# Optimization experiments

Measured on AMD Instinct MI355X. Metric: run time of the kernel, lower is better.

Reference implementation:

```python
import jax, jax.numpy as jnp
import numpy as np

N_NODES = 50000
N_EDGES = 800000
F_IN = 128
HEADS = 4
C_OUT = 16
NEG_SLOPE = 0.2


def setup_inputs() -> dict:
    key = jax.random.key(0)
    k1, k2, k3, k4, k5 = jax.random.split(key, 5)
    x = jax.random.normal(k1, (N_NODES, F_IN), dtype=jnp.float32)
    edge_index = jax.random.randint(k2, (2, N_EDGES), 0, N_NODES, dtype=jnp.int64)
    W = jax.random.normal(k3, (F_IN, HEADS * C_OUT), dtype=jnp.float32) * (1.0 / np.sqrt(F_IN))
    att_src = jax.random.normal(k4, (HEADS, C_OUT), dtype=jnp.float32) * (1.0 / np.sqrt(C_OUT))
    att_dst = jax.random.normal(k5, (HEADS, C_OUT), dtype=jnp.float32) * (1.0 / np.sqrt(C_OUT))
    bias = jnp.zeros((HEADS * C_OUT,), dtype=jnp.float32)
    return {"x": x, "edge_index": edge_index, "W": W,
            "att_src": att_src, "att_dst": att_dst, "bias": bias}


def reference(x, edge_index, W, att_src, att_dst, bias):
    N = x.shape[0]
    H, C = att_src.shape
    # PyG GATConv default: add self-loops
    loop = jnp.arange(N, dtype=edge_index.dtype)
    ei = jnp.concatenate([edge_index, jnp.stack([loop, loop])], axis=1)  # [2, E+N]
    src, dst = ei[0], ei[1]

    h = (x @ W).reshape(N, H, C)                      # [N, H, C]
    a_src = jnp.einsum('nhc,hc->nh', h, att_src)      # [N, H]
    a_dst = jnp.einsum('nhc,hc->nh', h, att_dst)      # [N, H]

    e = a_src[src] + a_dst[dst]                       # [E+N, H]
    e = jnp.where(e > 0, e, NEG_SLOPE * e)            # leaky_relu(0.2)

    # segment softmax over destination node (every segment has a self-loop)
    m = jax.ops.segment_max(e, dst, num_segments=N)   # [N, H]
    e = jnp.exp(e - m[dst])
    s = jax.ops.segment_sum(e, dst, num_segments=N)   # [N, H]
    alpha = e / (s[dst] + 1e-16)                      # [E+N, H]

    # scatter-aggregate weighted neighbor features
    out = jax.ops.segment_sum(h[src] * alpha[..., None], dst, num_segments=N)  # [N, H, C]
    out = out.reshape(N, H * C) + bias                # concat heads + bias
    return out, alpha
```

## Files before the change

### kernel.cpp

```cpp
#include <hip/hip_runtime.h>

#define N_NODES 50000
#define N_EDGES 800000
#define EN      (N_EDGES + N_NODES)
#define F_IN    128
#define HC      64
#define NEG_SLOPE 0.2f
#define NBUCK   196
#define BCAP    5120
#define P3_EPB  4096
#define LIN_BLOCKS 782
#define NBLK    196
#define RCAP    64
#define NSLOT   (NBLK * RCAP)
#define XPAD    136

typedef __attribute__((ext_vector_type(8))) short bf16x8;
typedef __attribute__((ext_vector_type(4))) float f32x4;

static __device__ __forceinline__ unsigned short f2bf(float f) {
    unsigned int b = __float_as_uint(f);
    return (unsigned short)((b + 0x7FFFu + ((b >> 16) & 1u)) >> 16);
}

__global__ __launch_bounds__(256) void
kA_linear_bin(const float* __restrict__ x, const float* __restrict__ W,
              const float* __restrict__ att_src, const float* __restrict__ att_dst,
              const int* __restrict__ ei,
              unsigned short* __restrict__ hbf, float* __restrict__ a_src,
              float* __restrict__ a_dst, int* __restrict__ bins,
              int* __restrict__ cntg) {
    __shared__ unsigned short xs[64][XPAD];
    __shared__ unsigned short wt[80][XPAD];
    __shared__ int bcnt_l[NBUCK];
    const int tid = threadIdx.x;

    if (blockIdx.x >= LIN_BLOCKS) {
        const int blk = blockIdx.x - LIN_BLOCKS;
        for (int i = tid; i < NBUCK; i += 256) bcnt_l[i] = 0;
        __syncthreads();
        const int base = blk * P3_EPB;
        #pragma unroll
        for (int j = 0; j < 16; ++j) {
            int i = base + j * 256 + tid;
            if (i < N_EDGES) {
                int sv = ei[i];
                int d  = ei[N_EDGES + i];
                int bk = d >> 8;
                int r  = atomicAdd(&bcnt_l[bk], 1);
                if (r < RCAP)
                    bins[(bk * NBLK + blk) * RCAP + r] = sv | ((d & 255) << 16);
            }
        }
        __syncthreads();
        for (int b = tid; b < NBUCK; b += 256)
            cntg[b * NBLK + blk] = min(bcnt_l[b], RCAP);
        return;
    }

    const int wv   = tid >> 6;
    const int l    = tid & 63;
    const int base = blockIdx.x * 64;
    const int c16  = l & 15;
    const int grp  = l >> 4;

    #pragma unroll
    for (int it = 0; it < 8; ++it) {
        int f  = it * 1024 + tid * 4;
        int k  = f >> 6;
        int cl = f & 63;
        float4 v = *(const float4*)(W + (size_t)k * HC + cl);
        wt[cl + 0][k] = f2bf(v.x);
        wt[cl + 1][k] = f2bf(v.y);
        wt[cl + 2][k] = f2bf(v.z);
        wt[cl + 3][k] = f2bf(v.w);
    }

    #pragma unroll
    for (int it = 0; it < 8; ++it) {
        int f   = it * 1024 + tid * 4;
        int row = f >> 7, k = f & 127;
        int gr  = base + row;
        float4 v = {0.f, 0.f, 0.f, 0.f};
        if (gr < N_NODES) v = *(const float4*)(x + (size_t)gr * F_IN + k);
        ushort4 u = {f2bf(v.x), f2bf(v.y), f2bf(v.z), f2bf(v.w)};
        *(ushort4*)(&xs[row][k]) = u;
    }

    {
        const int wk = tid >> 1;
        const int wo = (tid & 1) * 4;
        const float* wrow = W + (size_t)wk * HC;
        #pragma unroll
        for (int oo = 0; oo < 4; ++oo) {
            const int o = wo + oo;
            const int h = o & 3;
            const float* av = (o < 4) ? (att_src + h * 16) : (att_dst + h * 16);
            float a = 0.f;
            #pragma unroll
            for (int c = 0; c < 16; c += 4) {
                float4 w4 = *(const float4*)(wrow + h * 16 + c);
                float4 a4 = *(const float4*)(av + c);
                a += w4.x * a4.x + w4.y * a4.y + w4.z * a4.z + w4.w * a4.w;
            }
            wt[64 + o][wk] = f2bf(a);
        }
    }
    __syncthreads();

    bf16x8 Bf[5][4];
    #pragma unroll
    for (int t = 0; t < 5; ++t)
        #pragma unroll
        for (int kk = 0; kk < 4; ++kk)
            Bf[t][kk] = *(const bf16x8*)(&wt[t * 16 + c16][kk * 32 + grp * 8]);

    const int r0 = wv * 16;
    f32x4 C[4], C4;
    #pragma unroll
    for (int t = 0; t < 4; ++t) C[t] = (f32x4){0.f, 0.f, 0.f, 0.f};
    C4 = (f32x4){0.f, 0.f, 0.f, 0.f};
    bf16x8 A[4];
    #pragma unroll
    for (int kk = 0; kk < 4; ++kk)
        A[kk] = *(const bf16x8*)(&xs[r0 + c16][kk * 32 + grp * 8]);
    #pragma unroll
    for (int t = 0; t < 4; ++t)
        #pragma unroll
        for (int kk = 0; kk < 4; ++kk)
            C[t] = __builtin_amdgcn_mfma_f32_16x16x32_bf16(A[kk], Bf[t][kk], C[t], 0, 0, 0);
    #pragma unroll
    for (int kk = 0; kk < 4; ++kk)
        C4 = __builtin_amdgcn_mfma_f32_16x16x32_bf16(A[kk], Bf[4][kk], C4, 0, 0, 0);

    #pragma unroll
    for (int j = 0; j < 4; ++j) {
        const int row = base + r0 + grp * 4 + j;
        if (row < N_NODES) {
            #pragma unroll
            for (int t = 0; t < 4; ++t)
                hbf[(size_t)row * HC + t * 16 + c16] = f2bf(C[t][j]);
            if (c16 < 4)      a_src[row * 4 + c16]       = C4[j];
            else if (c16 < 8) a_dst[row * 4 + (c16 - 4)] = C4[j];
        }
    }
}

__global__ __launch_bounds__(256) void
p4_csr(const int* __restrict__ bins, const int* __restrict__ cntg,
       int* __restrict__ row_info, int* __restrict__ srcs) {
    __shared__ int psum[256];
    __shared__ int cnt[256], sm[256], cur[256];
    const int b = blockIdx.x, tid = threadIdx.x;
    const int node = (b << 8) + tid;

    psum[tid] = (tid < NBLK) ? cntg[b * NBLK + tid] : 0;
    cnt[tid] = (node < N_NODES) ? 1 : 0;
    __syncthreads();
    for (int off = 1; off < 256; off <<= 1) {
        int t = (tid >= off) ? psum[tid - off] : 0;
        __syncthreads();
        psum[tid] += t;
        __syncthreads();
    }
    const int T = psum[255];
    const int* bb = bins + (size_t)b * NSLOT;

    int pvs[20];
    #pragma unroll
    for (int it = 0; it < 20; ++it) {
        const int i = tid + it * 256;
        if (i < T) {
            int lo = 0, hi = NBLK - 1;
            while (lo < hi) { int mid = (lo + hi) >> 1;
                              if (psum[mid] > i) hi = mid; else lo = mid + 1; }
            const int k  = i - (lo ? psum[lo - 1] : 0);
            const int pv = bb[lo * RCAP + k];
            pvs[it] = pv;
            atomicAdd(&cnt[pv >> 16], 1);
        }
    }
    __syncthreads();

    int v = cnt[tid];
    sm[tid] = v;
    __syncthreads();
    for (int off = 1; off < 256; off <<= 1) {
        int t = (tid >= off) ? sm[tid - off] : 0;
        __syncthreads();
        sm[tid] += t;
        __syncthreads();
    }
    const int ex = sm[tid] - v;
    const int sbase = b * BCAP;

    if (node < N_NODES) {
        row_info[node] = ((sbase + ex) << 8) | v;
        srcs[sbase + ex] = node;
    }
    cur[tid] = ex + 1;
    __syncthreads();
    #pragma unroll
    for (int it = 0; it < 20; ++it) {
        const int i = tid + it * 256;
        if (i < T) {
            const int pv = pvs[it];
            const int p  = atomicAdd(&cur[pv >> 16], 1);
            srcs[sbase + p] = pv & 0xFFFF;
        }
    }
}

__global__ __launch_bounds__(256) void
k_agg(const int* __restrict__ row_info, const int* __restrict__ srcs,
      const float* __restrict__ a_src, const float* __restrict__ a_dst,
      const unsigned int* __restrict__ hw,
      const float* __restrict__ bias, float* __restrict__ out,
      float* __restrict__ s_inv) {
    __shared__ int   s_lds[4][4][16];
    __shared__ float p_lds[4][4][16][4];

    const int tid  = threadIdx.x;
    const int wv   = tid >> 6;
    const int lane = tid & 63;
    const int g    = lane >> 4;
    const int l    = lane & 15;
    const int hd   = l >> 2;
    const int d    = blockIdx.x * 16 + wv * 4 + g;

    const int info   = row_info[d];
    const int begin  = info >> 8;
    const int cnt    = info & 255;
    const int nchunk = (cnt + 15) >> 4;
    const float4 ad  = *(const float4*)(a_dst + d * 4);

    float4 ps = {0.f, 0.f, 0.f, 0.f};
    float a0 = 0.f, a1 = 0.f, a2 = 0.f, a3 = 0.f;

    for (int c = 0; c < nchunk; ++c) {
        const int k0 = begin + c * 16;
        const int m  = min(16, begin + cnt - k0);
        const int s = srcs[k0 + (l < m ? l : m - 1)];
        float4 p = {0.f, 0.f, 0.f, 0.f};
        if (l < m) {
            float4 as = *(const float4*)(a_src + s * 4);
            float e0 = as.x + ad.x, e1 = as.y + ad.y, e2 = as.z + ad.z, e3 = as.w + ad.w;
            e0 = e0 > 0.f ? e0 : NEG_SLOPE * e0;
            e1 = e1 > 0.f ? e1 : NEG_SLOPE * e1;
            e2 = e2 > 0.f ? e2 : NEG_SLOPE * e2;
            e3 = e3 > 0.f ? e3 : NEG_SLOPE * e3;
            p.x = __expf(e0); p.y = __expf(e1); p.z = __expf(e2); p.w = __expf(e3);
            ps.x += p.x; ps.y += p.y; ps.z += p.z; ps.w += p.w;
        }
        s_lds[wv][g][l] = s;
        *(float4*)(&p_lds[wv][g][l][0]) = p;
        __threadfence_block();

        const int mp = (m + 3) & ~3;
        for (int e = 0; e < mp; e += 4) {
            int s0 = s_lds[wv][g][e + 0], s1 = s_lds[wv][g][e + 1];
            int s2 = s_lds[wv][g][e + 2], s3 = s_lds[wv][g][e + 3];
            float p0 = p_lds[wv][g][e + 0][hd], p1 = p_lds[wv][g][e + 1][hd];
            float p2 = p_lds[wv][g][e + 2][hd], p3 = p_lds[wv][g][e + 3][hd];
            uint2 u0 = *(const uint2*)(hw + (size_t)s0 * 32 + l * 2);
            uint2 u1 = *(const uint2*)(hw + (size_t)s1 * 32 + l * 2);
            uint2 u2 = *(const uint2*)(hw + (size_t)s2 * 32 + l * 2);
            uint2 u3 = *(const uint2*)(hw + (size_t)s3 * 32 + l * 2);
            a0 += __uint_as_float(u0.x << 16)         * p0;
            a1 += __uint_as_float(u0.x & 0xFFFF0000u) * p0;
            a2 += __uint_as_float(u0.y << 16)         * p0;
            a3 += __uint_as_float(u0.y & 0xFFFF0000u) * p0;
            a0 += __uint_as_float(u1.x << 16)         * p1;
            a1 += __uint_as_float(u1.x & 0xFFFF0000u) * p1;
            a2 += __uint_as_float(u1.y << 16)         * p1;
            a3 += __uint_as_float(u1.y & 0xFFFF0000u) * p1;
            a0 += __uint_as_float(u2.x << 16)         * p2;
            a1 += __uint_as_float(u2.x & 0xFFFF0000u) * p2;
            a2 += __uint_as_float(u2.y << 16)         * p2;
            a3 += __uint_as_float(u2.y & 0xFFFF0000u) * p2;
            a0 += __uint_as_float(u3.x << 16)         * p3;
            a1 += __uint_as_float(u3.x & 0xFFFF0000u) * p3;
            a2 += __uint_as_float(u3.y << 16)         * p3;
            a3 += __uint_as_float(u3.y & 0xFFFF0000u) * p3;
        }
        __threadfence_block();
    }

    #pragma unroll
    for (int mm = 1; mm < 16; mm <<= 1) {
        ps.x += __shfl_xor(ps.x, mm);
        ps.y += __shfl_xor(ps.y, mm);
        ps.z += __shfl_xor(ps.z, mm);
        ps.w += __shfl_xor(ps.w, mm);
    }
    const float4 inv = {1.f / (ps.x + 1e-16f), 1.f / (ps.y + 1e-16f),
                        1.f / (ps.z + 1e-16f), 1.f / (ps.w + 1e-16f)};
    if (l == 0) *(float4*)(s_inv + d * 4) = inv;

    const float invh = (hd == 0) ? inv.x : (hd == 1) ? inv.y : (hd == 2) ? inv.z : inv.w;
    float4 o;
    o.x = a0 * invh + bias[l * 4 + 0];
    o.y = a1 * invh + bias[l * 4 + 1];
    o.z = a2 * invh + bias[l * 4 + 2];
    o.w = a3 * invh + bias[l * 4 + 3];
    *(float4*)(out + (size_t)d * HC + l * 4) = o;
}

__global__ void k_alpha(const int* __restrict__ ei, const float* __restrict__ a_src,
                        const float* __restrict__ a_dst, const float* __restrict__ s_inv,
                        float* __restrict__ alpha_out) {
    int i2 = blockIdx.x * 256 + threadIdx.x;
    if (i2 >= EN / 2) return;
    const int i = i2 * 2;
    int s0, s1, d0, d1;
    if (i < N_EDGES) {
        int2 sp = *(const int2*)(ei + i);
        int2 dp = *(const int2*)(ei + N_EDGES + i);
        s0 = sp.x; s1 = sp.y; d0 = dp.x; d1 = dp.y;
    } else {
        s0 = d0 = i - N_EDGES;
        s1 = d1 = i + 1 - N_EDGES;
    }

    float4 as0 = *(const float4*)(a_src + s0 * 4);
    float4 ad0 = *(const float4*)(a_dst + d0 * 4);
    float4 iv0 = *(const float4*)(s_inv + d0 * 4);
    float4 as1 = *(const float4*)(a_src + s1 * 4);
    float4 ad1 = *(const float4*)(a_dst + d1 * 4);
    float4 iv1 = *(const float4*)(s_inv + d1 * 4);

    float e0, e1, e2, e3;
    e0 = as0.x + ad0.x; e1 = as0.y + ad0.y; e2 = as0.z + ad0.z; e3 = as0.w + ad0.w;
    e0 = e0 > 0.f ? e0 : NEG_SLOPE * e0;
    e1 = e1 > 0.f ? e1 : NEG_SLOPE * e1;
    e2 = e2 > 0.f ? e2 : NEG_SLOPE * e2;
    e3 = e3 > 0.f ? e3 : NEG_SLOPE * e3;
    float4 al0 = {__expf(e0) * iv0.x, __expf(e1) * iv0.y,
                  __expf(e2) * iv0.z, __expf(e3) * iv0.w};
    e0 = as1.x + ad1.x; e1 = as1.y + ad1.y; e2 = as1.z + ad1.z; e3 = as1.w + ad1.w;
    e0 = e0 > 0.f ? e0 : NEG_SLOPE * e0;
    e1 = e1 > 0.f ? e1 : NEG_SLOPE * e1;
    e2 = e2 > 0.f ? e2 : NEG_SLOPE * e2;
    e3 = e3 > 0.f ? e3 : NEG_SLOPE * e3;
    float4 al1 = {__expf(e0) * iv1.x, __expf(e1) * iv1.y,
                  __expf(e2) * iv1.z, __expf(e3) * iv1.w};

    *(float4*)(alpha_out + (size_t)i * 4)     = al0;
    *(float4*)(alpha_out + (size_t)i * 4 + 4) = al1;
}

extern "C" void kernel_launch(void* const* d_in, const int* in_sizes, int n_in,
                              void* d_out, int out_size, void* d_ws, size_t ws_size,
                              hipStream_t stream) {
    const float* x       = (const float*)d_in[0];
    const int*   ei      = (const int*)d_in[1];
    const float* W       = (const float*)d_in[2];
    const float* att_src = (const float*)d_in[3];
    const float* att_dst = (const float*)d_in[4];
    const float* bias    = (const float*)d_in[5];

    float* out       = (float*)d_out;
    float* alpha_out = (float*)d_out + (size_t)N_NODES * HC;

    char* ws = (char*)d_ws;
    size_t off = 0;
    unsigned short* hbf = (unsigned short*)(ws + off); off += (size_t)N_NODES * HC * 2;
    float* a_src   = (float*)(ws + off); off += (size_t)N_NODES * 4 * 4;
    float* a_dst   = (float*)(ws + off); off += (size_t)N_NODES * 4 * 4;
    float* s_inv   = (float*)(ws + off); off += (size_t)N_NODES * 4 * 4;
    int* row_info  = (int*)(ws + off);   off += (size_t)N_NODES * 4;
    int* srcs      = (int*)(ws + off);   off += (size_t)NBUCK * BCAP * 4;
    int* bins      = (int*)(ws + off);   off += (size_t)NBUCK * NSLOT * 4;
    int* cntg      = (int*)(ws + off);   off += (size_t)NBUCK * NBLK * 4;

    kA_linear_bin<<<LIN_BLOCKS + NBLK, 256, 0, stream>>>(x, W, att_src, att_dst, ei,
                                                         hbf, a_src, a_dst, bins, cntg);
    p4_csr<<<NBUCK, 256, 0, stream>>>(bins, cntg, row_info, srcs);
    k_agg<<<N_NODES / 16, 256, 0, stream>>>(row_info, srcs, a_src, a_dst,
                                            (const unsigned int*)hbf, bias, out, s_inv);
    k_alpha<<<(EN / 2 + 255) / 256, 256, 0, stream>>>(ei, a_src, a_dst, s_inv, alpha_out);
}
```

Measured before the change: 80.93 us.

## Fuse alpha computation into aggregation kernel by storing edge ids in CSR

```diff
diff --git a/kernel.cpp b/kernel.cpp
--- a/kernel.cpp
+++ b/kernel.cpp
@@ -44,12 +44,11 @@
         for (int j = 0; j < 16; ++j) {
             int i = base + j * 256 + tid;
             if (i < N_EDGES) {
-                int sv = ei[i];
                 int d  = ei[N_EDGES + i];
                 int bk = d >> 8;
                 int r  = atomicAdd(&bcnt_l[bk], 1);
                 if (r < RCAP)
-                    bins[(bk * NBLK + blk) * RCAP + r] = sv | ((d & 255) << 16);
+                    bins[(bk * NBLK + blk) * RCAP + r] = i | ((d & 255) << 24);
             }
         }
         __syncthreads();
@@ -148,7 +147,7 @@
 
 __global__ __launch_bounds__(256) void
 p4_csr(const int* __restrict__ bins, const int* __restrict__ cntg,
-       int* __restrict__ row_info, int* __restrict__ srcs) {
+       int* __restrict__ row_info, int* __restrict__ eids) {
     __shared__ int psum[256];
     __shared__ int cnt[256], sm[256], cur[256];
     const int b = blockIdx.x, tid = threadIdx.x;
@@ -177,7 +176,7 @@
             const int k  = i - (lo ? psum[lo - 1] : 0);
             const int pv = bb[lo * RCAP + k];
             pvs[it] = pv;
-            atomicAdd(&cnt[pv >> 16], 1);
+            atomicAdd(&cnt[((unsigned)pv) >> 24], 1);
         }
     }
     __syncthreads();
@@ -196,7 +195,7 @@
 
     if (node < N_NODES) {
         row_info[node] = ((sbase + ex) << 8) | v;
-        srcs[sbase + ex] = node;
+        eids[sbase + ex] = N_EDGES + node;
     }
     cur[tid] = ex + 1;
     __syncthreads();
@@ -205,18 +204,19 @@
         const int i = tid + it * 256;
         if (i < T) {
             const int pv = pvs[it];
-            const int p  = atomicAdd(&cur[pv >> 16], 1);
-            srcs[sbase + p] = pv & 0xFFFF;
+            const int p  = atomicAdd(&cur[((unsigned)pv) >> 24], 1);
+            eids[sbase + p] = pv & 0xFFFFFF;
         }
     }
 }
 
 __global__ __launch_bounds__(256) void
-k_agg(const int* __restrict__ row_info, const int* __restrict__ srcs,
+k_agg(const int* __restrict__ row_info, const int* __restrict__ eids,
+      const int* __restrict__ ei,
       const float* __restrict__ a_src, const float* __restrict__ a_dst,
       const unsigned int* __restrict__ hw,
       const float* __restrict__ bias, float* __restrict__ out,
-      float* __restrict__ s_inv) {
+      float* __restrict__ alpha_out) {
     __shared__ int   s_lds[4][4][16];
     __shared__ float p_lds[4][4][16][4];
 
@@ -240,7 +240,8 @@
     for (int c = 0; c < nchunk; ++c) {
         const int k0 = begin + c * 16;
         const int m  = min(16, begin + cnt - k0);
-        const int s = srcs[k0 + (l < m ? l : m - 1)];
+        const int eid = eids[k0 + (l < m ? l : m - 1)];
+        const int s   = (eid >= N_EDGES) ? (eid - N_EDGES) : ei[eid];
         float4 p = {0.f, 0.f, 0.f, 0.f};
         if (l < m) {
             float4 as = *(const float4*)(a_src + s * 4);
@@ -295,7 +296,6 @@
     }
     const float4 inv = {1.f / (ps.x + 1e-16f), 1.f / (ps.y + 1e-16f),
                         1.f / (ps.z + 1e-16f), 1.f / (ps.w + 1e-16f)};
-    if (l == 0) *(float4*)(s_inv + d * 4) = inv;
 
     const float invh = (hd == 0) ? inv.x : (hd == 1) ? inv.y : (hd == 2) ? inv.z : inv.w;
     float4 o;
@@ -304,49 +304,24 @@
     o.z = a2 * invh + bias[l * 4 + 2];
     o.w = a3 * invh + bias[l * 4 + 3];
     *(float4*)(out + (size_t)d * HC + l * 4) = o;
-}
-
-__global__ void k_alpha(const int* __restrict__ ei, const float* __restrict__ a_src,
-                        const float* __restrict__ a_dst, const float* __restrict__ s_inv,
-                        float* __restrict__ alpha_out) {
-    int i2 = blockIdx.x * 256 + threadIdx.x;
-    if (i2 >= EN / 2) return;
-    const int i = i2 * 2;
-    int s0, s1, d0, d1;
-    if (i < N_EDGES) {
-        int2 sp = *(const int2*)(ei + i);
-        int2 dp = *(const int2*)(ei + N_EDGES + i);
-        s0 = sp.x; s1 = sp.y; d0 = dp.x; d1 = dp.y;
-    } else {
-        s0 = d0 = i - N_EDGES;
-        s1 = d1 = i + 1 - N_EDGES;
-    }
-
-    float4 as0 = *(const float4*)(a_src + s0 * 4);
-    float4 ad0 = *(const float4*)(a_dst + d0 * 4);
-    float4 iv0 = *(const float4*)(s_inv + d0 * 4);
-    float4 as1 = *(const float4*)(a_src + s1 * 4);
-    float4 ad1 = *(const float4*)(a_dst + d1 * 4);
-    float4 iv1 = *(const float4*)(s_inv + d1 * 4);
-
-    float e0, e1, e2, e3;
-    e0 = as0.x + ad0.x; e1 = as0.y + ad0.y; e2 = as0.z + ad0.z; e3 = as0.w + ad0.w;
-    e0 = e0 > 0.f ? e0 : NEG_SLOPE * e0;
-    e1 = e1 > 0.f ? e1 : NEG_SLOPE * e1;
-    e2 = e2 > 0.f ? e2 : NEG_SLOPE * e2;
-    e3 = e3 > 0.f ? e3 : NEG_SLOPE * e3;
-    float4 al0 = {__expf(e0) * iv0.x, __expf(e1) * iv0.y,
-                  __expf(e2) * iv0.z, __expf(e3) * iv0.w};
-    e0 = as1.x + ad1.x; e1 = as1.y + ad1.y; e2 = as1.z + ad1.z; e3 = as1.w + ad1.w;
-    e0 = e0 > 0.f ? e0 : NEG_SLOPE * e0;
-    e1 = e1 > 0.f ? e1 : NEG_SLOPE * e1;
-    e2 = e2 > 0.f ? e2 : NEG_SLOPE * e2;
-    e3 = e3 > 0.f ? e3 : NEG_SLOPE * e3;
-    float4 al1 = {__expf(e0) * iv1.x, __expf(e1) * iv1.y,
-                  __expf(e2) * iv1.z, __expf(e3) * iv1.w};
-
-    *(float4*)(alpha_out + (size_t)i * 4)     = al0;
-    *(float4*)(alpha_out + (size_t)i * 4 + 4) = al1;
+
+    for (int c = 0; c < nchunk; ++c) {
+        const int k0 = begin + c * 16;
+        const int m  = min(16, begin + cnt - k0);
+        if (l < m) {
+            const int eid = eids[k0 + l];
+            const int s   = (eid >= N_EDGES) ? (eid - N_EDGES) : ei[eid];
+            float4 as = *(const float4*)(a_src + s * 4);
+            float e0 = as.x + ad.x, e1 = as.y + ad.y, e2 = as.z + ad.z, e3 = as.w + ad.w;
+            e0 = e0 > 0.f ? e0 : NEG_SLOPE * e0;
+            e1 = e1 > 0.f ? e1 : NEG_SLOPE * e1;
+            e2 = e2 > 0.f ? e2 : NEG_SLOPE * e2;
+            e3 = e3 > 0.f ? e3 : NEG_SLOPE * e3;
+            float4 al = {__expf(e0) * inv.x, __expf(e1) * inv.y,
+                         __expf(e2) * inv.z, __expf(e3) * inv.w};
+            *(float4*)(alpha_out + (size_t)eid * 4) = al;
+        }
+    }
 }
 
 extern "C" void kernel_launch(void* const* d_in, const int* in_sizes, int n_in,
@@ -367,16 +342,14 @@
     unsigned short* hbf = (unsigned short*)(ws + off); off += (size_t)N_NODES * HC * 2;
     float* a_src   = (float*)(ws + off); off += (size_t)N_NODES * 4 * 4;
     float* a_dst   = (float*)(ws + off); off += (size_t)N_NODES * 4 * 4;
-    float* s_inv   = (float*)(ws + off); off += (size_t)N_NODES * 4 * 4;
     int* row_info  = (int*)(ws + off);   off += (size_t)N_NODES * 4;
-    int* srcs      = (int*)(ws + off);   off += (size_t)NBUCK * BCAP * 4;
+    int* eids      = (int*)(ws + off);   off += (size_t)NBUCK * BCAP * 4;
     int* bins      = (int*)(ws + off);   off += (size_t)NBUCK * NSLOT * 4;
     int* cntg      = (int*)(ws + off);   off += (size_t)NBUCK * NBLK * 4;
 
     kA_linear_bin<<<LIN_BLOCKS + NBLK, 256, 0, stream>>>(x, W, att_src, att_dst, ei,
                                                          hbf, a_src, a_dst, bins, cntg);
-    p4_csr<<<NBUCK, 256, 0, stream>>>(bins, cntg, row_info, srcs);
-    k_agg<<<N_NODES / 16, 256, 0, stream>>>(row_info, srcs, a_src, a_dst,
-                                            (const unsigned int*)hbf, bias, out, s_inv);
-    k_alpha<<<(EN / 2 + 255) / 256, 256, 0, stream>>>(ei, a_src, a_dst, s_inv, alpha_out);
-}
+    p4_csr<<<NBUCK, 256, 0, stream>>>(bins, cntg, row_info, eids);
+    k_agg<<<N_NODES / 16, 256, 0, stream>>>(row_info, eids, ei, a_src, a_dst,
+                                            (const unsigned int*)hbf, bias, out, alpha_out);
+}
```

New measurement: 90.45 us. +11.8%, slower.

## Assign one wavefront per destination node in aggregation kernel

Applied to the files above, without the earlier changes.

```diff
diff --git a/kernel.cpp b/kernel.cpp
--- a/kernel.cpp
+++ b/kernel.cpp
@@ -217,32 +217,31 @@
       const unsigned int* __restrict__ hw,
       const float* __restrict__ bias, float* __restrict__ out,
       float* __restrict__ s_inv) {
-    __shared__ int   s_lds[4][4][16];
-    __shared__ float p_lds[4][4][16][4];
+    __shared__ int   s_l[4][64];
+    __shared__ float p_l[4][64][4];
 
     const int tid  = threadIdx.x;
     const int wv   = tid >> 6;
     const int lane = tid & 63;
-    const int g    = lane >> 4;
-    const int l    = lane & 15;
-    const int hd   = l >> 2;
-    const int d    = blockIdx.x * 16 + wv * 4 + g;
-
-    const int info   = row_info[d];
-    const int begin  = info >> 8;
-    const int cnt    = info & 255;
-    const int nchunk = (cnt + 15) >> 4;
-    const float4 ad  = *(const float4*)(a_dst + d * 4);
+    const int g16  = lane >> 4;
+    const int c16  = lane & 15;
+    const int hd   = c16 >> 2;
+    const int d    = blockIdx.x * 4 + wv;
+
+    const int info  = row_info[d];
+    const int begin = info >> 8;
+    const int cnt   = info & 255;
+    const float4 ad = *(const float4*)(a_dst + d * 4);
 
     float4 ps = {0.f, 0.f, 0.f, 0.f};
     float a0 = 0.f, a1 = 0.f, a2 = 0.f, a3 = 0.f;
 
-    for (int c = 0; c < nchunk; ++c) {
-        const int k0 = begin + c * 16;
-        const int m  = min(16, begin + cnt - k0);
-        const int s = srcs[k0 + (l < m ? l : m - 1)];
+    for (int c0 = 0; c0 < cnt; c0 += 64) {
+        const int m = min(64, cnt - c0);
+        int s = d;
         float4 p = {0.f, 0.f, 0.f, 0.f};
-        if (l < m) {
+        if (lane < m) {
+            s = srcs[begin + c0 + lane];
             float4 as = *(const float4*)(a_src + s * 4);
             float e0 = as.x + ad.x, e1 = as.y + ad.y, e2 = as.z + ad.z, e3 = as.w + ad.w;
             e0 = e0 > 0.f ? e0 : NEG_SLOPE * e0;
@@ -252,42 +251,46 @@
             p.x = __expf(e0); p.y = __expf(e1); p.z = __expf(e2); p.w = __expf(e3);
             ps.x += p.x; ps.y += p.y; ps.z += p.z; ps.w += p.w;
         }
-        s_lds[wv][g][l] = s;
-        *(float4*)(&p_lds[wv][g][l][0]) = p;
+        s_l[wv][lane] = s;
+        *(float4*)(&p_l[wv][lane][0]) = p;
         __threadfence_block();
 
-        const int mp = (m + 3) & ~3;
-        for (int e = 0; e < mp; e += 4) {
-            int s0 = s_lds[wv][g][e + 0], s1 = s_lds[wv][g][e + 1];
-            int s2 = s_lds[wv][g][e + 2], s3 = s_lds[wv][g][e + 3];
-            float p0 = p_lds[wv][g][e + 0][hd], p1 = p_lds[wv][g][e + 1][hd];
-            float p2 = p_lds[wv][g][e + 2][hd], p3 = p_lds[wv][g][e + 3][hd];
-            uint2 u0 = *(const uint2*)(hw + (size_t)s0 * 32 + l * 2);
-            uint2 u1 = *(const uint2*)(hw + (size_t)s1 * 32 + l * 2);
-            uint2 u2 = *(const uint2*)(hw + (size_t)s2 * 32 + l * 2);
-            uint2 u3 = *(const uint2*)(hw + (size_t)s3 * 32 + l * 2);
-            a0 += __uint_as_float(u0.x << 16)         * p0;
-            a1 += __uint_as_float(u0.x & 0xFFFF0000u) * p0;
-            a2 += __uint_as_float(u0.y << 16)         * p0;
-            a3 += __uint_as_float(u0.y & 0xFFFF0000u) * p0;
-            a0 += __uint_as_float(u1.x << 16)         * p1;
-            a1 += __uint_as_float(u1.x & 0xFFFF0000u) * p1;
-            a2 += __uint_as_float(u1.y << 16)         * p1;
-            a3 += __uint_as_float(u1.y & 0xFFFF0000u) * p1;
-            a0 += __uint_as_float(u2.x << 16)         * p2;
-            a1 += __uint_as_float(u2.x & 0xFFFF0000u) * p2;
-            a2 += __uint_as_float(u2.y << 16)         * p2;
-            a3 += __uint_as_float(u2.y & 0xFFFF0000u) * p2;
-            a0 += __uint_as_float(u3.x << 16)         * p3;
-            a1 += __uint_as_float(u3.x & 0xFFFF0000u) * p3;
-            a2 += __uint_as_float(u3.y << 16)         * p3;
-            a3 += __uint_as_float(u3.y & 0xFFFF0000u) * p3;
+        const int mp16 = (m + 15) & ~15;
+        #pragma unroll
+        for (int eb = 0; eb < 4; ++eb) {
+            const int e = eb * 16;
+            if (e < mp16) {
+                int sA = s_l[wv][e + 0  + g16], sB = s_l[wv][e + 4  + g16];
+                int sC = s_l[wv][e + 8  + g16], sD = s_l[wv][e + 12 + g16];
+                float pA = p_l[wv][e + 0  + g16][hd], pB = p_l[wv][e + 4  + g16][hd];
+                float pC = p_l[wv][e + 8  + g16][hd], pD = p_l[wv][e + 12 + g16][hd];
+                uint2 uA = *(const uint2*)(hw + (size_t)sA * 32 + c16 * 2);
+                uint2 uB = *(const uint2*)(hw + (size_t)sB * 32 + c16 * 2);
+                uint2 uC = *(const uint2*)(hw + (size_t)sC * 32 + c16 * 2);
+                uint2 uD = *(const uint2*)(hw + (size_t)sD * 32 + c16 * 2);
+                a0 += __uint_as_float(uA.x << 16)         * pA;
+                a1 += __uint_as_float(uA.x & 0xFFFF0000u) * pA;
+                a2 += __uint_as_float(uA.y << 16)         * pA;
+                a3 += __uint_as_float(uA.y & 0xFFFF0000u) * pA;
+                a0 += __uint_as_float(uB.x << 16)         * pB;
+                a1 += __uint_as_float(uB.x & 0xFFFF0000u) * pB;
+                a2 += __uint_as_float(uB.y << 16)         * pB;
+                a3 += __uint_as_float(uB.y & 0xFFFF0000u) * pB;
+                a0 += __uint_as_float(uC.x << 16)         * pC;
+                a1 += __uint_as_float(uC.x & 0xFFFF0000u) * pC;
+                a2 += __uint_as_float(uC.y << 16)         * pC;
+                a3 += __uint_as_float(uC.y & 0xFFFF0000u) * pC;
+                a0 += __uint_as_float(uD.x << 16)         * pD;
+                a1 += __uint_as_float(uD.x & 0xFFFF0000u) * pD;
+                a2 += __uint_as_float(uD.y << 16)         * pD;
+                a3 += __uint_as_float(uD.y & 0xFFFF0000u) * pD;
+            }
         }
         __threadfence_block();
     }
 
     #pragma unroll
-    for (int mm = 1; mm < 16; mm <<= 1) {
+    for (int mm = 1; mm < 64; mm <<= 1) {
         ps.x += __shfl_xor(ps.x, mm);
         ps.y += __shfl_xor(ps.y, mm);
         ps.z += __shfl_xor(ps.z, mm);
@@ -295,15 +298,23 @@
     }
     const float4 inv = {1.f / (ps.x + 1e-16f), 1.f / (ps.y + 1e-16f),
                         1.f / (ps.z + 1e-16f), 1.f / (ps.w + 1e-16f)};
-    if (l == 0) *(float4*)(s_inv + d * 4) = inv;
-
-    const float invh = (hd == 0) ? inv.x : (hd == 1) ? inv.y : (hd == 2) ? inv.z : inv.w;
-    float4 o;
-    o.x = a0 * invh + bias[l * 4 + 0];
-    o.y = a1 * invh + bias[l * 4 + 1];
-    o.z = a2 * invh + bias[l * 4 + 2];
-    o.w = a3 * invh + bias[l * 4 + 3];
-    *(float4*)(out + (size_t)d * HC + l * 4) = o;
+    if (lane == 0) *(float4*)(s_inv + d * 4) = inv;
+
+    a0 += __shfl_xor(a0, 16); a0 += __shfl_xor(a0, 32);
+    a1 += __shfl_xor(a1, 16); a1 += __shfl_xor(a1, 32);
+    a2 += __shfl_xor(a2, 16); a2 += __shfl_xor(a2, 32);
+    a3 += __shfl_xor(a3, 16); a3 += __shfl_xor(a3, 32);
+
+    if (g16 == 0) {
+        const float invh = (hd == 0) ? inv.x : (hd == 1) ? inv.y
+                         : (hd == 2) ? inv.z : inv.w;
+        float4 o;
+        o.x = a0 * invh + bias[c16 * 4 + 0];
+        o.y = a1 * invh + bias[c16 * 4 + 1];
+        o.z = a2 * invh + bias[c16 * 4 + 2];
+        o.w = a3 * invh + bias[c16 * 4 + 3];
+        *(float4*)(out + (size_t)d * HC + c16 * 4) = o;
+    }
 }
 
 __global__ void k_alpha(const int* __restrict__ ei, const float* __restrict__ a_src,
@@ -376,7 +387,7 @@
     kA_linear_bin<<<LIN_BLOCKS + NBLK, 256, 0, stream>>>(x, W, att_src, att_dst, ei,
                                                          hbf, a_src, a_dst, bins, cntg);
     p4_csr<<<NBUCK, 256, 0, stream>>>(bins, cntg, row_info, srcs);
-    k_agg<<<N_NODES / 16, 256, 0, stream>>>(row_info, srcs, a_src, a_dst,
-                                            (const unsigned int*)hbf, bias, out, s_inv);
+    k_agg<<<12500, 256, 0, stream>>>(row_info, srcs, a_src, a_dst,
+                                     (const unsigned int*)hbf, bias, out, s_inv);
     k_alpha<<<(EN / 2 + 255) / 256, 256, 0, stream>>>(ei, a_src, a_dst, s_inv, alpha_out);
 }
```

Measured after the change: 87.71 us. 1.08x slower.

## Split aggregation by head with head-major bf16 feature layout

Applied to the files above, without the earlier changes.

```diff
diff --git a/kernel.cpp b/kernel.cpp
--- a/kernel.cpp
+++ b/kernel.cpp
@@ -14,6 +14,7 @@
 #define RCAP    64
 #define NSLOT   (NBLK * RCAP)
 #define XPAD    136
+#define DGRP    782
 
 typedef __attribute__((ext_vector_type(8))) short bf16x8;
 typedef __attribute__((ext_vector_type(4))) float f32x4;
@@ -139,7 +140,7 @@
         if (row < N_NODES) {
             #pragma unroll
             for (int t = 0; t < 4; ++t)
-                hbf[(size_t)row * HC + t * 16 + c16] = f2bf(C[t][j]);
+                hbf[((size_t)t * N_NODES + row) * 16 + c16] = f2bf(C[t][j]);
             if (c16 < 4)      a_src[row * 4 + c16]       = C4[j];
             else if (c16 < 8) a_dst[row * 4 + (c16 - 4)] = C4[j];
         }
@@ -212,98 +213,61 @@
 }
 
 __global__ __launch_bounds__(256) void
-k_agg(const int* __restrict__ row_info, const int* __restrict__ srcs,
-      const float* __restrict__ a_src, const float* __restrict__ a_dst,
-      const unsigned int* __restrict__ hw,
-      const float* __restrict__ bias, float* __restrict__ out,
-      float* __restrict__ s_inv) {
-    __shared__ int   s_lds[4][4][16];
-    __shared__ float p_lds[4][4][16][4];
-
+k_aggh(const int* __restrict__ row_info, const int* __restrict__ srcs,
+       const float* __restrict__ a_src, const float* __restrict__ a_dst,
+       const unsigned int* __restrict__ hw,
+       const float* __restrict__ bias, float* __restrict__ out,
+       float* __restrict__ s_inv) {
     const int tid  = threadIdx.x;
-    const int wv   = tid >> 6;
-    const int lane = tid & 63;
-    const int g    = lane >> 4;
-    const int l    = lane & 15;
-    const int hd   = l >> 2;
-    const int d    = blockIdx.x * 16 + wv * 4 + g;
-
-    const int info   = row_info[d];
-    const int begin  = info >> 8;
-    const int cnt    = info & 255;
-    const int nchunk = (cnt + 15) >> 4;
-    const float4 ad  = *(const float4*)(a_dst + d * 4);
-
-    float4 ps = {0.f, 0.f, 0.f, 0.f};
+    const int bid  = blockIdx.x;
+    const int head = bid / DGRP;
+    const int grp  = bid % DGRP;
+    const int q    = tid & 3;
+    const int d    = grp * 64 + (tid >> 2);
+    if (d >= N_NODES) return;
+
+    const int info  = row_info[d];
+    const int begin = info >> 8;
+    const int cnt   = info & 255;
+    const float adh = a_dst[d * 4 + head];
+    const unsigned int* __restrict__ hwh = hw + (size_t)head * N_NODES * 8;
+
+    float ps = 0.f;
     float a0 = 0.f, a1 = 0.f, a2 = 0.f, a3 = 0.f;
 
-    for (int c = 0; c < nchunk; ++c) {
-        const int k0 = begin + c * 16;
-        const int m  = min(16, begin + cnt - k0);
-        const int s = srcs[k0 + (l < m ? l : m - 1)];
-        float4 p = {0.f, 0.f, 0.f, 0.f};
-        if (l < m) {
-            float4 as = *(const float4*)(a_src + s * 4);
-            float e0 = as.x + ad.x, e1 = as.y + ad.y, e2 = as.z + ad.z, e3 = as.w + ad.w;
-            e0 = e0 > 0.f ? e0 : NEG_SLOPE * e0;
-            e1 = e1 > 0.f ? e1 : NEG_SLOPE * e1;
-            e2 = e2 > 0.f ? e2 : NEG_SLOPE * e2;
-            e3 = e3 > 0.f ? e3 : NEG_SLOPE * e3;
-            p.x = __expf(e0); p.y = __expf(e1); p.z = __expf(e2); p.w = __expf(e3);
-            ps.x += p.x; ps.y += p.y; ps.z += p.z; ps.w += p.w;
-        }
-        s_lds[wv][g][l] = s;
-        *(float4*)(&p_lds[wv][g][l][0]) = p;
-        __threadfence_block();
-
-        const int mp = (m + 3) & ~3;
-        for (int e = 0; e < mp; e += 4) {
-            int s0 = s_lds[wv][g][e + 0], s1 = s_lds[wv][g][e + 1];
-            int s2 = s_lds[wv][g][e + 2], s3 = s_lds[wv][g][e + 3];
-            float p0 = p_lds[wv][g][e + 0][hd], p1 = p_lds[wv][g][e + 1][hd];
-            float p2 = p_lds[wv][g][e + 2][hd], p3 = p_lds[wv][g][e + 3][hd];
-            uint2 u0 = *(const uint2*)(hw + (size_t)s0 * 32 + l * 2);
-            uint2 u1 = *(const uint2*)(hw + (size_t)s1 * 32 + l * 2);
-            uint2 u2 = *(const uint2*)(hw + (size_t)s2 * 32 + l * 2);
-            uint2 u3 = *(const uint2*)(hw + (size_t)s3 * 32 + l * 2);
-            a0 += __uint_as_float(u0.x << 16)         * p0;
-            a1 += __uint_as_float(u0.x & 0xFFFF0000u) * p0;
-            a2 += __uint_as_float(u0.y << 16)         * p0;
-            a3 += __uint_as_float(u0.y & 0xFFFF0000u) * p0;
-            a0 += __uint_as_float(u1.x << 16)         * p1;
-            a1 += __uint_as_float(u1.x & 0xFFFF0000u) * p1;
-            a2 += __uint_as_float(u1.y << 16)         * p1;
-            a3 += __uint_as_float(u1.y & 0xFFFF0000u) * p1;
-            a0 += __uint_as_float(u2.x << 16)         * p2;
-            a1 += __uint_as_float(u2.x & 0xFFFF0000u) * p2;
-            a2 += __uint_as_float(u2.y << 16)         * p2;
-            a3 += __uint_as_float(u2.y & 0xFFFF0000u) * p2;
-            a0 += __uint_as_float(u3.x << 16)         * p3;
-            a1 += __uint_as_float(u3.x & 0xFFFF0000u) * p3;
-            a2 += __uint_as_float(u3.y << 16)         * p3;
-            a3 += __uint_as_float(u3.y & 0xFFFF0000u) * p3;
-        }
-        __threadfence_block();
-    }
-
-    #pragma unroll
-    for (int mm = 1; mm < 16; mm <<= 1) {
-        ps.x += __shfl_xor(ps.x, mm);
-        ps.y += __shfl_xor(ps.y, mm);
-        ps.z += __shfl_xor(ps.z, mm);
-        ps.w += __shfl_xor(ps.w, mm);
-    }
-    const float4 inv = {1.f / (ps.x + 1e-16f), 1.f / (ps.y + 1e-16f),
-                        1.f / (ps.z + 1e-16f), 1.f / (ps.w + 1e-16f)};
-    if (l == 0) *(float4*)(s_inv + d * 4) = inv;
-
-    const float invh = (hd == 0) ? inv.x : (hd == 1) ? inv.y : (hd == 2) ? inv.z : inv.w;
+    for (int c0 = 0; c0 < cnt; c0 += 4) {
+        const int j = c0 + q;
+        const int s = srcs[begin + (j < cnt ? j : cnt - 1)];
+        float p = 0.f;
+        if (j < cnt) {
+            float e = a_src[s * 4 + head] + adh;
+            e = e > 0.f ? e : NEG_SLOPE * e;
+            p = __expf(e);
+            ps += p;
+        }
+        #pragma unroll
+        for (int jj = 0; jj < 4; ++jj) {
+            const int   sj = __shfl(s, jj, 4);
+            const float pj = __shfl(p, jj, 4);
+            uint2 u = *(const uint2*)(hwh + (size_t)sj * 8 + q * 2);
+            a0 += __uint_as_float(u.x << 16)         * pj;
+            a1 += __uint_as_float(u.x & 0xFFFF0000u) * pj;
+            a2 += __uint_as_float(u.y << 16)         * pj;
+            a3 += __uint_as_float(u.y & 0xFFFF0000u) * pj;
+        }
+    }
+
+    ps += __shfl_xor(ps, 1);
+    ps += __shfl_xor(ps, 2);
+    const float inv = 1.f / (ps + 1e-16f);
+    if (q == 0) s_inv[d * 4 + head] = inv;
+
     float4 o;
-    o.x = a0 * invh + bias[l * 4 + 0];
-    o.y = a1 * invh + bias[l * 4 + 1];
-    o.z = a2 * invh + bias[l * 4 + 2];
-    o.w = a3 * invh + bias[l * 4 + 3];
-    *(float4*)(out + (size_t)d * HC + l * 4) = o;
+    o.x = a0 * inv + bias[head * 16 + q * 4 + 0];
+    o.y = a1 * inv + bias[head * 16 + q * 4 + 1];
+    o.z = a2 * inv + bias[head * 16 + q * 4 + 2];
+    o.w = a3 * inv + bias[head * 16 + q * 4 + 3];
+    *(float4*)(out + (size_t)d * HC + head * 16 + q * 4) = o;
 }
 
 __global__ void k_alpha(const int* __restrict__ ei, const float* __restrict__ a_src,
@@ -376,7 +340,7 @@
     kA_linear_bin<<<LIN_BLOCKS + NBLK, 256, 0, stream>>>(x, W, att_src, att_dst, ei,
                                                          hbf, a_src, a_dst, bins, cntg);
     p4_csr<<<NBUCK, 256, 0, stream>>>(bins, cntg, row_info, srcs);
-    k_agg<<<N_NODES / 16, 256, 0, stream>>>(row_info, srcs, a_src, a_dst,
-                                            (const unsigned int*)hbf, bias, out, s_inv);
+    k_aggh<<<DGRP * 4, 256, 0, stream>>>(row_info, srcs, a_src, a_dst,
+                                         (const unsigned int*)hbf, bias, out, s_inv);
     k_alpha<<<(EN / 2 + 255) / 256, 256, 0, stream>>>(ei, a_src, a_dst, s_inv, alpha_out);
 }
```

Measured after the change: 105.1 us. 29.8% more time.
